# Performance work log

Measured on AMD Instinct MI355X. Metric: run time of the kernel, lower is better.

The kernel has to match this reference:

```python
import jax, jax.numpy as jnp
import numpy as np

EPS = 1e-12  # F.normalize default eps


def _unfold(x, k, pad, stride):
    # torch F.unfold: [B,C,H,W] -> [B, C*k*k, L], features ordered (c, kh, kw), L row-major.
    B, C, H, W = x.shape
    xp = jnp.pad(x, ((0, 0), (0, 0), (pad, pad), (pad, pad)))
    Ho = (H + 2 * pad - k) // stride + 1
    Wo = (W + 2 * pad - k) // stride + 1
    r = (jnp.arange(Ho) * stride)[:, None] + jnp.arange(k)[None, :]  # [Ho,k]
    c = (jnp.arange(Wo) * stride)[:, None] + jnp.arange(k)[None, :]  # [Wo,k]
    p = xp[:, :, r[:, None, :, None], c[None, :, None, :]]  # [B,C,Ho,Wo,k,k]
    return p.transpose(0, 1, 4, 5, 2, 3).reshape(B, C * k * k, Ho * Wo)


def _fold(p, out_hw, k, pad, stride):
    # torch F.fold: overlap-add inverse of _unfold.
    B, CKK, L = p.shape
    C = CKK // (k * k)
    H, W = out_hw
    Ho = (H + 2 * pad - k) // stride + 1
    Wo = (W + 2 * pad - k) // stride + 1
    p = p.reshape(B, C, k, k, Ho, Wo).transpose(0, 1, 4, 5, 2, 3)  # [B,C,Ho,Wo,k,k]
    r = (jnp.arange(Ho) * stride)[:, None] + jnp.arange(k)[None, :]
    c = (jnp.arange(Wo) * stride)[:, None] + jnp.arange(k)[None, :]
    out = jnp.zeros((B, C, H + 2 * pad, W + 2 * pad), p.dtype)
    out = out.at[:, :, r[:, None, :, None], c[None, :, None, :]].add(p)
    return out[:, :, pad:pad + H, pad:pad + W]


def _l2n(x, axis):
    n = jnp.sqrt(jnp.sum(x * x, axis=axis, keepdims=True))
    return x / jnp.maximum(n, EPS)


def setup_inputs() -> dict:
    key = jax.random.key(0)
    ks = jax.random.split(key, 11)
    B, H, W = 1, 32, 32
    f = jnp.float32
    return {
        'lrsr_lv3': jax.random.normal(ks[0], (B, 256, H, W), f),
        'refsr_lv1': jax.random.normal(ks[1], (B, 64, 4 * H, 4 * W), f),
        'refsr_lv2': jax.random.normal(ks[2], (B, 128, 2 * H, 2 * W), f),
        'refsr_lv3': jax.random.normal(ks[3], (B, 256, H, W), f),
        'ref_lv1': jax.random.normal(ks[4], (B, 64, 4 * H, 4 * W), f),
        'ref_lv2': jax.random.normal(ks[5], (B, 128, 2 * H, 2 * W), f),
        'ref_lv3': jax.random.normal(ks[6], (B, 256, H, W), f),
        'W1': jax.random.normal(ks[7], (2304, 1152), f) * 0.02,
        'b1': jax.random.normal(ks[8], (2304,), f) * 0.02,
        'W2': jax.random.normal(ks[9], (2304, 576), f) * 0.02,
        'b2': jax.random.normal(ks[10], (2304,), f) * 0.02,
    }


def reference(lrsr_lv3, refsr_lv1, refsr_lv2, refsr_lv3, ref_lv1, ref_lv2, ref_lv3, W1, b1, W2, b2):
    B, _, H, W = lrsr_lv3.shape
    lr3 = _unfold(lrsr_lv3, 3, 1, 1)                       # [B, 2304, N]
    r3 = _unfold(refsr_lv3, 3, 1, 1).transpose(0, 2, 1)    # [B, N3, 2304]
    r2 = _unfold(refsr_lv2, 3, 1, 1).transpose(0, 2, 1) @ W1.T + b1  # [B, N2, 2304]
    r1 = _unfold(refsr_lv1, 3, 1, 1).transpose(0, 2, 1) @ W2.T + b2  # [B, N1, 2304]
    r3 = _l2n(r3, 2); r2 = _l2n(r2, 2); r1 = _l2n(r1, 2)
    lr3 = _l2n(lr3, 1)
    R3 = jnp.einsum('bnd,bdm->bnm', r3, lr3)  # [B, N3, N]
    R2 = jnp.einsum('bnd,bdm->bnm', r2, lr3)  # [B, N2, N]
    R1 = jnp.einsum('bnd,bdm->bnm', r1, lr3)  # [B, N1, N]
    R3_star = jnp.max(R3, axis=1); R3_arg = jnp.argmax(R3, axis=1)
    R2_star = jnp.max(R2, axis=1)
    R1_star = jnp.max(R1, axis=1)
    ref3u = _unfold(ref_lv3, 3, 1, 1)
    ref2u = _unfold(ref_lv2, 6, 2, 2)
    ref1u = _unfold(ref_lv1, 12, 4, 4)
    idx = R3_arg[:, None, :]  # [B,1,N] broadcast over feature dim
    T3u = jnp.take_along_axis(ref3u, idx, axis=2)
    T2u = jnp.take_along_axis(ref2u, idx, axis=2)
    T1u = jnp.take_along_axis(ref1u, idx, axis=2)
    T_lv3 = _fold(T3u, (H, W), 3, 1, 1) / 9.0
    T_lv2 = _fold(T2u, (2 * H, 2 * W), 6, 2, 2) / 9.0
    T_lv1 = _fold(T1u, (4 * H, 4 * W), 12, 4, 4) / 9.0
    S_3 = R3_star.reshape(B, 1, H, W)
    S_2 = R2_star.reshape(B, 1, H, W)
    S_1 = R1_star.reshape(B, 1, H, W)
    return (S_1, S_2, S_3, T_lv3, T_lv2, T_lv1)
```

## Files before the change

### kernel.cpp

```cpp
#include <hip/hip_runtime.h>

typedef short bf8 __attribute__((ext_vector_type(8)));
typedef float f32x4 __attribute__((ext_vector_type(4)));

static __device__ __forceinline__ unsigned short f2bf(float f) {
  unsigned u = __float_as_uint(f);
  unsigned r = u + 0x7FFFu + ((u >> 16) & 1u);
  return (unsigned short)(r >> 16);
}
static __device__ __forceinline__ float bf2f(unsigned short h) {
  return __uint_as_float(((unsigned)h) << 16);
}
static __device__ __forceinline__ unsigned fkey(float f) {
  unsigned u = __float_as_uint(f);
  return (u & 0x80000000u) ? ~u : (u | 0x80000000u);
}
static __device__ __forceinline__ float kdec(unsigned k) {
  unsigned u = (k & 0x80000000u) ? (k & 0x7FFFFFFFu) : ~k;
  return __uint_as_float(u);
}
static __device__ __forceinline__ int xcdswz(int h, int nwg) {
  int q = nwg >> 3, r = nwg & 7;
  int xcd = h & 7, w = h >> 3;
  return (xcd < r ? xcd * (q + 1) : r * (q + 1) + (xcd - r) * q) + w;
}
static __device__ __forceinline__ int xcdbal(int h, int nwg, int nb0) {
  int xcd = h & 7, w = h >> 3;
  int qa = nb0 >> 3, qb = (nwg - nb0) >> 3;
  return (w < qa) ? (xcd * qa + w) : (nb0 + xcd * qb + (w - qa));
}
static __device__ __forceinline__ float win9s(const float* __restrict__ b, int m) {
  int mi = m >> 5, mj = m & 31;
  float s = 0.f;
#pragma unroll
  for (int dy = -1; dy <= 1; ++dy) {
    int i = mi + dy; if ((unsigned)i >= 32u) continue;
#pragma unroll
    for (int dx = -1; dx <= 1; ++dx) {
      int jx = mj + dx; if ((unsigned)jx >= 32u) continue;
      s += b[i * 32 + jx];
    }
  }
  return s;
}

static __device__ __forceinline__ void gload_lds16(const unsigned short* g, unsigned short* l) {
  __builtin_amdgcn_global_load_lds((const __attribute__((address_space(1))) void*)g,
                                   (__attribute__((address_space(3))) void*)l, 16, 0, 0);
}

static __device__ __forceinline__ float uf3(const float* __restrict__ src, int lgS, int d, int m) {
  const int S = 1 << lgS;
  int cc = d / 9;
  int r9 = d - cc * 9;
  int ki = r9 / 3;
  int kj = r9 - ki * 3;
  int i = (m >> lgS) + ki - 1;
  int j = (m & (S - 1)) + kj - 1;
  if ((unsigned)i >= (unsigned)S || (unsigned)j >= (unsigned)S) return 0.f;
  return src[((size_t)cc << (2 * lgS)) + ((size_t)i << lgS) + j];
}

__global__ __launch_bounds__(256) void k_prepA(const float* __restrict__ lrsr3, const float* __restrict__ rsr3,
                                               const float* __restrict__ rsr2, const float* __restrict__ rsr1,
                                               const float* __restrict__ W1, const float* __restrict__ W2,
                                               const float* __restrict__ b1, const float* __restrict__ b2,
                                               float* __restrict__ G2,
                                               float* __restrict__ rsr2t, float* __restrict__ rsr1t,
                                               unsigned short* __restrict__ lr3nbT,
                                               unsigned short* __restrict__ W1t, unsigned short* __restrict__ W2t,
                                               float* __restrict__ sclw, float* __restrict__ scu3w,
                                               float* __restrict__ D1, float* __restrict__ D2) {
  __shared__ __align__(16) unsigned char smem[18432];
  const int blk = blockIdx.x;
  const int tid = threadIdx.x;
  if (blk < 4) {
    float* b1L = (float*)smem;
    float* b2L = b1L + 2304;
    const int p = blk * 256 + tid;
    for (int i = tid; i < 2304; i += 256) { b1L[i] = b1[i]; b2L[i] = b2[i]; }
    __syncthreads();
    float d1a[9] = {}, d2a[9] = {};
    for (int cc = 0; cc < 256; ++cc) {
      float v = lrsr3[(size_t)cc * 1024 + p];
#pragma unroll
      for (int kk = 0; kk < 9; ++kk) {
        d1a[kk] = fmaf(b1L[cc * 9 + kk], v, d1a[kk]);
        d2a[kk] = fmaf(b2L[cc * 9 + kk], v, d2a[kk]);
      }
    }
#pragma unroll
    for (int kk = 0; kk < 9; ++kk) { D1[kk * 1024 + p] = d1a[kk]; D2[kk * 1024 + p] = d2a[kk]; }
  } else if (blk < 6) {
    float* ss = (float*)smem;
    const float* src = (blk == 4) ? lrsr3 : rsr3;
    float a4[4] = {0.f, 0.f, 0.f, 0.f};
    for (int cc = 0; cc < 256; ++cc) {
#pragma unroll
      for (int k = 0; k < 4; ++k) {
        float v = src[(size_t)cc * 1024 + k * 256 + tid];
        a4[k] = fmaf(v, v, a4[k]);
      }
    }
#pragma unroll
    for (int k = 0; k < 4; ++k) ss[k * 256 + tid] = a4[k];
    __syncthreads();
    float* dst = (blk == 4) ? sclw : scu3w;
#pragma unroll
    for (int k = 0; k < 4; ++k) {
      int m = k * 256 + tid;
      dst[m] = 1.f / fmaxf(sqrtf(win9s(ss, m)), 1e-12f);
    }
  } else if (blk < 1030) {
    float (*As)[32] = (float(*)[32])smem;
    float (*Bs)[32] = (float(*)[32])(smem + 2048);
    const int px = blk - 6;
    const int m0 = (px >> 5) * 32, n0 = (px & 31) * 32;
    const int tx = tid & 15, ty = tid >> 4;
    float acc[2][2] = {};
    for (int kb = 0; kb < 256; kb += 16) {
      __syncthreads();
      {
        int kk = tid >> 5, mm = tid & 31;
        As[kk][mm] = lrsr3[(size_t)(kb + kk) * 1024 + m0 + mm];
        Bs[kk][mm] = rsr3[(size_t)(kb + kk) * 1024 + n0 + mm];
        int e2 = tid + 256; int kk2 = e2 >> 5, mm2 = e2 & 31;
        As[kk2][mm2] = lrsr3[(size_t)(kb + kk2) * 1024 + m0 + mm2];
        Bs[kk2][mm2] = rsr3[(size_t)(kb + kk2) * 1024 + n0 + mm2];
      }
      __syncthreads();
#pragma unroll
      for (int kk = 0; kk < 16; ++kk) {
        float a0 = As[kk][ty * 2], a1 = As[kk][ty * 2 + 1];
        float b0 = Bs[kk][tx * 2], b1v = Bs[kk][tx * 2 + 1];
        acc[0][0] = fmaf(a0, b0, acc[0][0]); acc[0][1] = fmaf(a0, b1v, acc[0][1]);
        acc[1][0] = fmaf(a1, b0, acc[1][0]); acc[1][1] = fmaf(a1, b1v, acc[1][1]);
      }
    }
#pragma unroll
    for (int i = 0; i < 2; ++i)
#pragma unroll
      for (int jj = 0; jj < 2; ++jj)
        G2[(size_t)(m0 + ty * 2 + i) * 1024 + (n0 + tx * 2 + jj)] = acc[i][jj];
  } else if (blk < 1158) {
    float (*Tt)[65] = (float(*)[65])smem;
    const int idx = blk - 1030;
    const int ct = idx & 1, st = idx >> 1;
#pragma unroll
    for (int i = 0; i < 16; ++i) {
      int id = tid + i * 256;
      int r = id >> 6, c = id & 63;
      Tt[r][c] = rsr2[(size_t)(ct * 64 + r) * 4096 + st * 64 + c];
    }
    __syncthreads();
#pragma unroll
    for (int i = 0; i < 16; ++i) {
      int id = tid + i * 256;
      int cc2 = id >> 6, rr = id & 63;
      rsr2t[(size_t)(st * 64 + cc2) * 128 + ct * 64 + rr] = Tt[rr][cc2];
    }
  } else if (blk < 1414) {
    float (*Tt)[65] = (float(*)[65])smem;
    const int st = blk - 1158;
#pragma unroll
    for (int i = 0; i < 16; ++i) {
      int id = tid + i * 256;
      int r = id >> 6, c = id & 63;
      Tt[r][c] = rsr1[(size_t)r * 16384 + st * 64 + c];
    }
    __syncthreads();
#pragma unroll
    for (int i = 0; i < 16; ++i) {
      int id = tid + i * 256;
      int cc2 = id >> 6, rr = id & 63;
      rsr1t[(size_t)(st * 64 + cc2) * 64 + rr] = Tt[rr][cc2];
    }
  } else if (blk < 2566) {
    int id8 = (blk - 1414) * 256 + tid;
    int m = id8 / 288, c0 = (id8 - m * 288) * 8;
    bf8 v;
#pragma unroll
    for (int e = 0; e < 8; ++e) v[e] = (short)f2bf(uf3(lrsr3, 5, c0 + e, m));
    *(bf8*)(lr3nbT + (size_t)m * 2304 + c0) = v;
  } else {
    unsigned short (*Ls)[65] = (unsigned short(*)[65])smem;
    int idx = blk - 2566;
    int xx = idx % 27, yy = idx / 27;
    const float* W; unsigned short* Wt; int Cw, c0;
    if (xx < 18) { W = W1; Wt = W1t; Cw = 1152; c0 = xx * 64; }
    else         { W = W2; Wt = W2t; Cw = 576;  c0 = (xx - 18) * 64; }
    const int Cch = Cw / 9;
    const int d0 = yy * 64;
#pragma unroll
    for (int i = 0; i < 16; ++i) {
      int id = tid + i * 256;
      int r = id >> 6, c = id & 63;
      Ls[r][c] = f2bf(W[(size_t)(d0 + r) * Cw + c0 + c]);
    }
    __syncthreads();
#pragma unroll
    for (int i = 0; i < 16; ++i) {
      int id = tid + i * 256;
      int cc = id >> 6, rr = id & 63;
      int c = c0 + cc;
      Wt[(size_t)((c % 9) * Cch + c / 9) * 2304 + d0 + rr] = Ls[rr][cc];
    }
  }
}

struct Job {
  const unsigned short* Alo;
  const unsigned short* Ahi;
  const unsigned short* Bt;
  unsigned short* Clo;
  unsigned short* Chi;
  const float* bl;
  const float* bw;
  const float* bbp;
  const float* rowscale;
  float* pnsq;
  float* pbwd;
  float* cmax;
  int Msplit, N, K, nbx, Mtot, npart, which;
};

template <int EPI, int NBUF>
static __device__ __forceinline__ void gemm_body(const Job& j0, const Job& j1, int nb0, int bid,
                                                 unsigned char* smem) {
  unsigned short (*As)[128 * 64] = (unsigned short(*)[128 * 64])smem;
  unsigned short (*Bs)[128 * 64] = (unsigned short(*)[128 * 64])(smem + (size_t)NBUF * 16384);
  unsigned* colkey = (unsigned*)(smem + (size_t)2 * NBUF * 16384);
  float* ninvL = (float*)(smem + (size_t)2 * NBUF * 16384 + 512);

  const bool first = (bid < nb0);
  const Job j = first ? j0 : j1;
  const int local = bid - (first ? 0 : nb0);
  const int by = local / j.nbx;
  const int bx = local - by * j.nbx;
  const int m0 = by * 128, n0 = bx * 128;
  const int K = j.K, N = j.N;

  const unsigned short* Abase = (m0 < j.Msplit)
      ? j.Alo + (size_t)m0 * K
      : j.Ahi + (size_t)(m0 - j.Msplit) * K;

  const int tid = threadIdx.x;
  const int l = tid & 63;
  const int w = tid >> 6;
  const int wr = w >> 1, wc = w & 1;
  if (EPI == 2) {
    if (tid < 128) {
      colkey[tid] = 0u;
      const int r = m0 + tid;
      float nsq = 0.f, bwd = 0.f;
      for (int p = 0; p < j.npart; ++p) {
        nsq += j.pnsq[(size_t)p * j.Mtot + r];
        bwd += j.pbwd[(size_t)p * j.Mtot + r];
      }
      float tq = nsq + 2.f * bwd + j.bbp[j.which];
      ninvL[tid] = 1.f / fmaxf(sqrtf(fmaxf(tq, 0.f)), 1e-12f);
    }
  }

  f32x4 acc[4][4] = {};

  const int srow = w * 32;
  const int lrow = l >> 3;
  const int gcol = ((l & 7) ^ lrow) * 8;
  const int mr = l & 15;
  const int kg = l >> 4;

  const int nt = K >> 6;
  const int snap_kb = n0 + wc * 64;
  unsigned short snap[4][4][4];

  auto stage = [&](int buf, int kb) {
#pragma unroll
    for (int i = 0; i < 4; ++i) {
      int r = srow + i * 8;
      gload_lds16(Abase + (size_t)(r + lrow) * K + kb + gcol, &As[buf][r * 64]);
      gload_lds16(j.Bt + (size_t)(n0 + r + lrow) * K + kb + gcol, &Bs[buf][r * 64]);
    }
  };
  auto compute_tile = [&](int cur) {
#pragma unroll
    for (int ks = 0; ks < 2; ++ks) {
      bf8 af[4], bv[4];
#pragma unroll
      for (int mi = 0; mi < 4; ++mi) {
        const int row = wr * 64 + mi * 16 + mr;
        af[mi] = *(const bf8*)&As[cur][row * 64 + (((ks * 4 + kg) ^ (row & 7)) * 8)];
      }
#pragma unroll
      for (int ni = 0; ni < 4; ++ni) {
        const int row = wc * 64 + ni * 16 + mr;
        bv[ni] = *(const bf8*)&Bs[cur][row * 64 + (((ks * 4 + kg) ^ (row & 7)) * 8)];
      }
      __builtin_amdgcn_s_setprio(1);
#pragma unroll
      for (int mi = 0; mi < 4; ++mi)
#pragma unroll
        for (int ni = 0; ni < 4; ++ni)
          acc[mi][ni] = __builtin_amdgcn_mfma_f32_16x16x32_bf16(af[mi], bv[ni], acc[mi][ni], 0, 0, 0);
      __builtin_amdgcn_s_setprio(0);
    }
  };
  auto do_snap = [&](int cur) {
#pragma unroll
    for (int mi = 0; mi < 4; ++mi)
#pragma unroll
      for (int e = 0; e < 4; ++e) {
        const int row = wr * 64 + mi * 16 + kg * 4 + e;
#pragma unroll
        for (int ni = 0; ni < 4; ++ni) {
          const int slot = ni * 2 + (mr >> 3);
          snap[mi][ni][e] = As[cur][row * 64 + ((slot ^ (row & 7)) * 8) + (mr & 7)];
        }
      }
  };

  if constexpr (NBUF == 1) {
    for (int t = 0; t < nt; ++t) {
      if (t) __syncthreads();
      stage(0, t << 6);
      __syncthreads();
      compute_tile(0);
      if (EPI == 1 && (t << 6) == snap_kb) do_snap(0);
    }
  } else {
    auto waitv = [&](int Wt) {
      if (Wt >= 2)      asm volatile("s_waitcnt vmcnt(16)\ns_barrier" ::: "memory");
      else if (Wt == 1) asm volatile("s_waitcnt vmcnt(8)\ns_barrier" ::: "memory");
      else              asm volatile("s_waitcnt vmcnt(0)\ns_barrier" ::: "memory");
    };
#pragma unroll
    for (int p = 0; p < NBUF; ++p) if (p < nt) stage(p, p << 6);
    { int inflight = (NBUF < nt ? NBUF : nt); waitv(inflight - 1); }
    int cur = 0;
    for (int t = 0; t < nt; ++t) {
      compute_tile(cur);
      if (EPI == 1 && (t << 6) == snap_kb) do_snap(cur);
      if (t + 1 < nt) {
        asm volatile("s_waitcnt lgkmcnt(0)\ns_barrier" ::: "memory");
        if (t + NBUF < nt) stage(cur, (t + NBUF) << 6);
        const int im = (nt - 1 < t + NBUF) ? (nt - 1) : (t + NBUF);
        waitv(im - (t + 1));
        cur = (cur + 1 == NBUF) ? 0 : cur + 1;
      }
    }
  }

  const int lr0 = wr * 64;
  const int lc0 = wc * 64;
  if (EPI == 0) {
    const bool hi = (m0 >= j.Msplit);
    unsigned short* Cbase = hi ? j.Chi + (size_t)(m0 - j.Msplit) * N
                               : j.Clo + (size_t)m0 * N;
    float rs[4][4];
#pragma unroll
    for (int mi = 0; mi < 4; ++mi)
#pragma unroll
      for (int e = 0; e < 4; ++e)
        rs[mi][e] = hi ? j.rowscale[m0 - j.Msplit + lr0 + mi * 16 + kg * 4 + e] : 1.f;
#pragma unroll
    for (int mi = 0; mi < 4; ++mi)
#pragma unroll
      for (int ni = 0; ni < 4; ++ni)
#pragma unroll
        for (int e = 0; e < 4; ++e)
          Cbase[(size_t)(lr0 + mi * 16 + kg * 4 + e) * (size_t)N + (n0 + lc0 + ni * 16 + mr)] =
              f2bf(acc[mi][ni][e] * rs[mi][e]);
  } else if (EPI == 1) {
    float rp[4][4] = {};
    float bp[4][4] = {};
#pragma unroll
    for (int ni = 0; ni < 4; ++ni) {
      const float bwv = j.bw[n0 + lc0 + ni * 16 + mr];
#pragma unroll
      for (int mi = 0; mi < 4; ++mi)
#pragma unroll
        for (int e = 0; e < 4; ++e) {
          const float av = bf2f(snap[mi][ni][e]);
          rp[mi][e] += acc[mi][ni][e] * av;
          bp[mi][e] += bwv * av;
        }
    }
#pragma unroll
    for (int off = 1; off < 16; off <<= 1)
#pragma unroll
      for (int mi = 0; mi < 4; ++mi)
#pragma unroll
        for (int e = 0; e < 4; ++e) {
          rp[mi][e] += __shfl_xor(rp[mi][e], off);
          bp[mi][e] += __shfl_xor(bp[mi][e], off);
        }
    if (mr == 0) {
      const size_t slotbase = (size_t)(bx * 2 + wc) * j.Mtot;
#pragma unroll
      for (int mi = 0; mi < 4; ++mi)
#pragma unroll
        for (int e = 0; e < 4; ++e) {
          const int r = m0 + lr0 + mi * 16 + kg * 4 + e;
          j.pnsq[slotbase + r] = rp[mi][e];
          j.pbwd[slotbase + r] = bp[mi][e];
        }
    }
  } else {
    float nv[4][4];
#pragma unroll
    for (int mi = 0; mi < 4; ++mi)
#pragma unroll
      for (int e = 0; e < 4; ++e)
        nv[mi][e] = ninvL[lr0 + mi * 16 + kg * 4 + e];
#pragma unroll
    for (int ni = 0; ni < 4; ++ni) {
      float blv = j.bl[n0 + lc0 + ni * 16 + mr];
      float mx = -3.0e38f;
#pragma unroll
      for (int mi = 0; mi < 4; ++mi)
#pragma unroll
        for (int e = 0; e < 4; ++e) mx = fmaxf(mx, (acc[mi][ni][e] + blv) * nv[mi][e]);
      atomicMax(&colkey[lc0 + ni * 16 + mr], fkey(mx));
    }
    __syncthreads();
    if (tid < 128) j.cmax[(size_t)by * 1024 + n0 + tid] = kdec(colkey[tid]);
  }
}

__global__ __launch_bounds__(256) void k_prepBP(Job pa, Job pb, int nbP0,
                                                const float* __restrict__ rsr2t, const float* __restrict__ rsr1t,
                                                const float* __restrict__ W1, const float* __restrict__ W2,
                                                const float* __restrict__ b1, const float* __restrict__ b2,
                                                const float* __restrict__ sclw, const float* __restrict__ scu3w,
                                                const float* __restrict__ D1, const float* __restrict__ D2,
                                                const float* __restrict__ G2,
                                                unsigned short* __restrict__ U2b, unsigned short* __restrict__ U1b,
                                                float* __restrict__ bw2, float* __restrict__ bw1,
                                                float* __restrict__ bb,
                                                float* __restrict__ bl2, float* __restrict__ bl1,
                                                float* __restrict__ s3, int* __restrict__ arg) {
  __shared__ __align__(16) unsigned char sm[33792];
  const int blk = blockIdx.x;
  const int tid = threadIdx.x;
  if (blk < 218) {
    gemm_body<0, 1>(pa, pb, nbP0, xcdswz(blk, 218), sm);
  } else if (blk < 2522) {
    int id = (blk - 218) * 256 + tid;
    int t = id & 15, rest = id >> 4;
    int kk = rest % 9, n = rest / 9;
    int cc0 = t * 8;
    int ki = kk / 3, kj = kk - ki * 3;
    int sy = (n >> 6) + ki - 1, sx = (n & 63) + kj - 1;
    bf8 v;
    if ((unsigned)sy < 64u && (unsigned)sx < 64u) {
      const float* p = rsr2t + (size_t)(sy * 64 + sx) * 128 + cc0;
      f32x4 a = *(const f32x4*)p;
      f32x4 bq = *(const f32x4*)(p + 4);
#pragma unroll
      for (int e = 0; e < 4; ++e) { v[e] = (short)f2bf(a[e]); v[4 + e] = (short)f2bf(bq[e]); }
    } else {
#pragma unroll
      for (int e = 0; e < 8; ++e) v[e] = 0;
    }
    *(bf8*)(U2b + (size_t)n * 1152 + kk * 128 + cc0) = v;
  } else if (blk < 7642) {
    int id = (blk - 2522) * 256 + tid;
    int n = id / 80, rem = id - n * 80;
    int ks = rem >> 3, t = rem & 7;
    int cc0 = t * 8;
    bf8 v;
    if (ks == 9) {
#pragma unroll
      for (int e = 0; e < 8; ++e) v[e] = 0;
    } else {
      int ki = ks / 3, kj = ks - ki * 3;
      int sy = (n >> 7) + ki - 1, sx = (n & 127) + kj - 1;
      if ((unsigned)sy < 128u && (unsigned)sx < 128u) {
        const float* p = rsr1t + (size_t)(sy * 128 + sx) * 64 + cc0;
        f32x4 a = *(const f32x4*)p;
        f32x4 bq = *(const f32x4*)(p + 4);
#pragma unroll
        for (int e = 0; e < 4; ++e) { v[e] = (short)f2bf(a[e]); v[4 + e] = (short)f2bf(bq[e]); }
      } else {
#pragma unroll
        for (int e = 0; e < 8; ++e) v[e] = 0;
      }
    }
    *(bf8*)(U1b + (size_t)n * 640 + ks * 64 + cc0) = v;
  } else if (blk < 7722) {
    float* red = (float*)sm;
    int idx = blk - 7642;
    int x = idx & 7, y = idx >> 3;
    if (y == 9) {
      if (x >= 2) return;
      const float* b = x ? b2 : b1;
      float s = 0.f;
      for (int d = tid; d < 2304; d += 256) s += b[d] * b[d];
      red[tid] = s; __syncthreads();
      for (int o = 128; o > 0; o >>= 1) { if (tid < o) red[tid] += red[tid + o]; __syncthreads(); }
      if (tid == 0) bb[x] = red[0];
      return;
    }
    const bool two = x < 5;
    const float* W = two ? W1 : W2;
    const float* b = two ? b1 : b2;
    float* bw = two ? bw2 : bw1;
    const int Cw = two ? 1152 : 576;
    int c = (two ? x : x - 5) * 256 + tid;
    if (c >= Cw) return;
    int d0 = y * 256;
    float s = 0.f;
    for (int d = d0; d < d0 + 256; ++d) s += b[d] * W[(size_t)d * Cw + c];
    atomicAdd(&bw[(c % 9) * (Cw / 9) + c / 9], s);
  } else if (blk < 8746) {
    float* bv = (float*)sm;
    int* bidx = (int*)(sm + 1024);
    const int m = blk - 7722;
    const int mi = m >> 5, mj = m & 31;
    float best = -3.0e38f; int bi = 0;
    for (int n = tid; n < 1024; n += 256) {
      const int ni = n >> 5, nj = n & 31;
      float raw = 0.f;
#pragma unroll
      for (int dy = -1; dy <= 1; ++dy) {
#pragma unroll
        for (int dx = -1; dx <= 1; ++dx) {
          bool vm = ((unsigned)(mi + dy) < 32u) && ((unsigned)(mj + dx) < 32u);
          bool vn = ((unsigned)(ni + dy) < 32u) && ((unsigned)(nj + dx) < 32u);
          if (vm && vn) {
            int off = dy * 32 + dx;
            raw += G2[(size_t)(m + off) * 1024 + (n + off)];
          }
        }
      }
      float v = raw * scu3w[n];
      if (v > best) { best = v; bi = n; }
    }
    bv[tid] = best; bidx[tid] = bi;
    __syncthreads();
    for (int o = 128; o > 0; o >>= 1) {
      if (tid < o) {
        float ov = bv[tid + o]; int oi = bidx[tid + o];
        if (ov > bv[tid] || (ov == bv[tid] && oi < bidx[tid])) { bv[tid] = ov; bidx[tid] = oi; }
      }
      __syncthreads();
    }
    if (tid == 0) { s3[m] = bv[0] * sclw[m]; arg[m] = bidx[0]; }
  } else {
    int m = (blk - 8746) * 256 + tid;
    int mi = m >> 5, mj = m & 31;
    float a1 = 0.f, a2 = 0.f;
#pragma unroll
    for (int ki = 0; ki < 3; ++ki) {
      int i = mi + ki - 1; if ((unsigned)i >= 32u) continue;
#pragma unroll
      for (int kj = 0; kj < 3; ++kj) {
        int jx = mj + kj - 1; if ((unsigned)jx >= 32u) continue;
        int pix = i * 32 + jx;
        int kk = ki * 3 + kj;
        a1 += D1[kk * 1024 + pix];
        a2 += D2[kk * 1024 + pix];
      }
    }
    float sc = sclw[m];
    bl2[m] = a1 * sc;
    bl1[m] = a2 * sc;
  }
}

__global__ __launch_bounds__(256) void k_gE1F(Job a, Job b, int nb0,
                                              const float* __restrict__ ref3, const float* __restrict__ ref2,
                                              const float* __restrict__ ref1, const int* __restrict__ arg,
                                              float* __restrict__ out) {
  __shared__ __align__(16) unsigned char sm[33792];
  const int bid = blockIdx.x;
  const int tid = threadIdx.x;
  if (bid < 928) {
    gemm_body<1, 1>(a, b, nb0, xcdbal(bid, 928, nb0), sm);
  } else if (bid < 1184) {
    float* plane = (float*)sm;
    int* argL = (int*)(sm + 4096);
    const int c = bid - 928;
#pragma unroll
    for (int k = 0; k < 4; ++k) {
      plane[k * 256 + tid] = ref3[(size_t)c * 1024 + k * 256 + tid];
      argL[k * 256 + tid] = arg[k * 256 + tid];
    }
    __syncthreads();
#pragma unroll
    for (int k = 0; k < 4; ++k) {
      int px = k * 256 + tid;
      int y = px >> 5, x = px & 31;
      float s = 0.f;
#pragma unroll
      for (int di = -1; di <= 1; ++di) {
        int i = y + di;
        if ((unsigned)i >= 32u) continue;
#pragma unroll
        for (int dj = -1; dj <= 1; ++dj) {
          int jw = x + dj;
          if ((unsigned)jw >= 32u) continue;
          int n2 = argL[i * 32 + jw];
          int rr = (n2 >> 5) + y - i, cc = (n2 & 31) + x - jw;
          if ((unsigned)rr < 32u && (unsigned)cc < 32u) s += plane[rr * 32 + cc];
        }
      }
      out[3072 + (size_t)c * 1024 + px] = s * (1.f / 9.f);
    }
  } else if (bid < 2208) {
    int* argL = (int*)sm;
#pragma unroll
    for (int k = 0; k < 4; ++k) argL[k * 256 + tid] = arg[k * 256 + tid];
    __syncthreads();
    int id2 = (bid - 1184) * 256 + tid;
    int q = id2 & 31, y = (id2 >> 5) & 63, c = id2 >> 11;
    int iy = y >> 1;
    float s0 = 0.f, s1 = 0.f;
#pragma unroll
    for (int di = -1; di <= 1; ++di) {
      int i = iy + di;
      if ((unsigned)i >= 32u) continue;
      int ry = y - 2 * i;
#pragma unroll
      for (int dj = -1; dj <= 1; ++dj) {
        int jw = q + dj;
        if ((unsigned)jw >= 32u) continue;
        int n2 = argL[i * 32 + jw];
        int rr = (n2 >> 5) * 2 + ry;
        int cb = (n2 & 31) * 2 + 2 * (q - jw);
        if ((unsigned)rr < 64u && (unsigned)cb < 63u) {
          const float* p = ref2 + (size_t)c * 4096 + rr * 64 + cb;
          s0 += p[0]; s1 += p[1];
        }
      }
    }
    float2 o; o.x = s0 * (1.f / 9.f); o.y = s1 * (1.f / 9.f);
    *(float2*)(out + 265216 + (size_t)c * 4096 + y * 64 + 2 * q) = o;
  } else {
    int* argL = (int*)sm;
#pragma unroll
    for (int k = 0; k < 4; ++k) argL[k * 256 + tid] = arg[k * 256 + tid];
    __syncthreads();
    int id1 = (bid - 2208) * 256 + tid;
    int q = id1 & 31, y = (id1 >> 5) & 127, c = id1 >> 12;
    int iy = y >> 2;
    f32x4 s = {0.f, 0.f, 0.f, 0.f};
#pragma unroll
    for (int di = -1; di <= 1; ++di) {
      int i = iy + di;
      if ((unsigned)i >= 32u) continue;
      int ry = y - 4 * i;
#pragma unroll
      for (int dj = -1; dj <= 1; ++dj) {
        int jw = q + dj;
        if ((unsigned)jw >= 32u) continue;
        int n2 = argL[i * 32 + jw];
        int rr = (n2 >> 5) * 4 + ry;
        int cb = (n2 & 31) * 4 + 4 * (q - jw);
        if ((unsigned)rr < 128u && (unsigned)cb < 125u) {
          f32x4 v = *(const f32x4*)(ref1 + (size_t)c * 16384 + rr * 128 + cb);
          s += v;
        }
      }
    }
    s *= (1.f / 9.f);
    *(f32x4*)(out + 789504 + (size_t)c * 16384 + y * 128 + 4 * q) = s;
  }
}

__global__ __launch_bounds__(256) void k_gE2(Job a, Job b, int nb0) {
  __shared__ __align__(16) unsigned char sm[33792];
  gemm_body<2, 1>(a, b, nb0, xcdbal((int)blockIdx.x, (int)gridDim.x, nb0), sm);
}

__global__ __launch_bounds__(256) void k_sfin(const float* __restrict__ cmax1, const float* __restrict__ cmax2,
                                              float* __restrict__ out) {
  int t = blockIdx.x * 256 + threadIdx.x;
  if (t < 1024) {
    float mx = -3.0e38f;
    for (int rb = 0; rb < 128; ++rb) mx = fmaxf(mx, cmax1[rb * 1024 + t]);
    out[t] = mx;
  } else {
    int tt = t - 1024;
    float mx = -3.0e38f;
    for (int rb = 0; rb < 32; ++rb) mx = fmaxf(mx, cmax2[rb * 1024 + tt]);
    out[1024 + tt] = mx;
  }
}

static constexpr size_t OFF_BW2     = 0;
static constexpr size_t OFF_BW1     = 4608;
static constexpr size_t ZERO_BYTES  = 7168;
static constexpr size_t OFF_BB      = 7168;
static constexpr size_t OFF_BL2     = 7424;
static constexpr size_t OFF_BL1     = 11520;
static constexpr size_t OFF_SCLW    = 15616;
static constexpr size_t OFF_SCU3W   = 19712;
static constexpr size_t OFF_R3ARG   = 23808;
static constexpr size_t OFF_PNSQ2   = 27904;
static constexpr size_t OFF_PBWD2   = OFF_PNSQ2 + 294912;
static constexpr size_t OFF_PNSQ1   = OFF_PBWD2 + 294912;
static constexpr size_t OFF_PBWD1   = OFF_PNSQ1 + 655360;
static constexpr size_t OFF_CMAX2   = OFF_PBWD1 + 655360;
static constexpr size_t OFF_CMAX1   = OFF_CMAX2 + 131072;
static constexpr size_t OFF_LR3NBT  = OFF_CMAX1 + 524288;
static constexpr size_t OFF_U2B     = OFF_LR3NBT + 4718592;
static constexpr size_t OFF_U1B     = OFF_U2B    + 9437184;
static constexpr size_t OFF_W1T     = OFF_U1B    + 20971520;
static constexpr size_t OFF_W2T     = OFF_W1T    + 5308416;
static constexpr size_t OFF_A2      = OFF_W2T    + 2949120;
static constexpr size_t OFF_A1      = OFF_A2     + 2654208;
static constexpr size_t OFF_M2T     = OFF_A1     + 819200;
static constexpr size_t OFF_M1T     = OFF_M2T    + 2359296;
static constexpr size_t OFF_G2      = OFF_M1T    + 1310720;
static constexpr size_t OFF_R2T     = OFF_G2     + 4194304;
static constexpr size_t OFF_R1T     = OFF_R2T    + 2097152;
static constexpr size_t OFF_D1      = OFF_R1T    + 4194304;
static constexpr size_t OFF_D2      = OFF_D1     + 36864;

extern "C" void kernel_launch(void* const* d_in, const int* in_sizes, int n_in,
                              void* d_out, int out_size, void* d_ws, size_t ws_size,
                              hipStream_t stream) {
  (void)in_sizes; (void)n_in; (void)out_size; (void)ws_size;
  const float* lrsr3  = (const float*)d_in[0];
  const float* rsr1   = (const float*)d_in[1];
  const float* rsr2   = (const float*)d_in[2];
  const float* rsr3   = (const float*)d_in[3];
  const float* ref1   = (const float*)d_in[4];
  const float* ref2   = (const float*)d_in[5];
  const float* ref3   = (const float*)d_in[6];
  const float* W1     = (const float*)d_in[7];
  const float* b1     = (const float*)d_in[8];
  const float* W2     = (const float*)d_in[9];
  const float* b2     = (const float*)d_in[10];
  float* out = (float*)d_out;
  char* ws = (char*)d_ws;

  float*          bw2     = (float*)(ws + OFF_BW2);
  float*          bw1     = (float*)(ws + OFF_BW1);
  float*          bb      = (float*)(ws + OFF_BB);
  float*          bl2     = (float*)(ws + OFF_BL2);
  float*          bl1     = (float*)(ws + OFF_BL1);
  float*          sclw    = (float*)(ws + OFF_SCLW);
  float*          scu3w   = (float*)(ws + OFF_SCU3W);
  int*            R3arg   = (int*)(ws + OFF_R3ARG);
  float*          pnsq2   = (float*)(ws + OFF_PNSQ2);
  float*          pbwd2   = (float*)(ws + OFF_PBWD2);
  float*          pnsq1   = (float*)(ws + OFF_PNSQ1);
  float*          pbwd1   = (float*)(ws + OFF_PBWD1);
  float*          cmax2   = (float*)(ws + OFF_CMAX2);
  float*          cmax1   = (float*)(ws + OFF_CMAX1);
  unsigned short* lr3nbT  = (unsigned short*)(ws + OFF_LR3NBT);
  unsigned short* U2b     = (unsigned short*)(ws + OFF_U2B);
  unsigned short* U1b     = (unsigned short*)(ws + OFF_U1B);
  unsigned short* W1t     = (unsigned short*)(ws + OFF_W1T);
  unsigned short* W2t     = (unsigned short*)(ws + OFF_W2T);
  unsigned short* A2b     = (unsigned short*)(ws + OFF_A2);
  unsigned short* A1b     = (unsigned short*)(ws + OFF_A1);
  unsigned short* M2tb    = (unsigned short*)(ws + OFF_M2T);
  unsigned short* M1tb    = (unsigned short*)(ws + OFF_M1T);
  float*          G2      = (float*)(ws + OFF_G2);
  float*          rsr2t   = (float*)(ws + OFF_R2T);
  float*          rsr1t   = (float*)(ws + OFF_R1T);
  float*          D1      = (float*)(ws + OFF_D1);
  float*          D2      = (float*)(ws + OFF_D2);

  hipMemsetAsync(d_ws, 0, ZERO_BYTES, stream);
  hipMemsetAsync(ws + OFF_W2T + (size_t)576 * 2304 * 2, 0, (size_t)64 * 2304 * 2, stream);

  k_prepA<<<3538, 256, 0, stream>>>(lrsr3, rsr3, rsr2, rsr1, W1, W2, b1, b2,
                                    G2, rsr2t, rsr1t, lr3nbT, W1t, W2t, sclw, scu3w, D1, D2);

  Job jz = {};
  {
    Job a = jz, b = jz;
    a.Alo = W1t; a.Ahi = lr3nbT; a.Msplit = 1152; a.Bt = W1t;
    a.Clo = A2b; a.Chi = M2tb; a.rowscale = sclw; a.N = 1152; a.K = 2304; a.nbx = 9;
    b.Alo = W2t; b.Ahi = lr3nbT; b.Msplit = 640; b.Bt = W2t;
    b.Clo = A1b; b.Chi = M1tb; b.rowscale = sclw; b.N = 640; b.K = 2304; b.nbx = 5;
    k_prepBP<<<8750, 256, 0, stream>>>(a, b, 153, rsr2t, rsr1t, W1, W2, b1, b2,
                                       sclw, scu3w, D1, D2, G2,
                                       U2b, U1b, bw2, bw1, bb, bl2, bl1, out + 2048, R3arg);
  }
  {
    Job a = jz, b = jz;
    a.Alo = U2b; a.Ahi = U2b; a.Msplit = 4096; a.Bt = A2b;
    a.bw = bw2; a.pnsq = pnsq2; a.pbwd = pbwd2; a.Mtot = 4096;
    a.N = 1152; a.K = 1152; a.nbx = 9;
    b.Alo = U1b; b.Ahi = U1b; b.Msplit = 16384; b.Bt = A1b;
    b.bw = bw1; b.pnsq = pnsq1; b.pbwd = pbwd1; b.Mtot = 16384;
    b.N = 640; b.K = 640; b.nbx = 5;
    k_gE1F<<<3232, 256, 0, stream>>>(a, b, 288, ref3, ref2, ref1, R3arg, out);
  }
  {
    Job a = jz, b = jz;
    a.Alo = U2b; a.Ahi = U2b; a.Msplit = 4096; a.Bt = M2tb;
    a.bl = bl2; a.pnsq = pnsq2; a.pbwd = pbwd2; a.bbp = bb;
    a.npart = 18; a.which = 0; a.cmax = cmax2; a.Mtot = 4096;
    a.N = 1024; a.K = 1152; a.nbx = 8;
    b.Alo = U1b; b.Ahi = U1b; b.Msplit = 16384; b.Bt = M1tb;
    b.bl = bl1; b.pnsq = pnsq1; b.pbwd = pbwd1; b.bbp = bb;
    b.npart = 10; b.which = 1; b.cmax = cmax1; b.Mtot = 16384;
    b.N = 1024; b.K = 640; b.nbx = 8;
    k_gE2<<<256 + 1024, 256, 0, stream>>>(a, b, 256);
  }

  k_sfin<<<8, 256, 0, stream>>>(cmax1, cmax2, out);
}
```

Before: 208.9 us.

## Split-K the weight Gram GEMM in prepBP with fp32 atomics and a combine kernel

The K=2304 weight-product GEMM inside k_prepBP is split into two K halves, doubling its block count from 218 to 436, to raise parallelism for this long-K tail. Each half atomically adds fp32 partials into a new zeroed workspace. A new k_pcomb kernel then applies the row scale and converts to bf16 for the downstream GEMMs. In exchange it adds a memset of about 14 MB, atomic traffic, an extra kernel launch and fp32 partial reads and writes. It also removes the unused multi-buffer pipeline path from gemm_body.

```diff
diff --git a/kernel.cpp b/kernel.cpp
--- a/kernel.cpp
+++ b/kernel.cpp
@@ -212,21 +212,19 @@
   const unsigned short* Alo;
   const unsigned short* Ahi;
   const unsigned short* Bt;
-  unsigned short* Clo;
-  unsigned short* Chi;
   const float* bl;
   const float* bw;
   const float* bbp;
-  const float* rowscale;
+  float* Fp;
   float* pnsq;
   float* pbwd;
   float* cmax;
-  int Msplit, N, K, nbx, Mtot, npart, which;
+  int Msplit, N, K, Kst, nbx, Mtot, npart, which;
 };
 
 template <int EPI, int NBUF>
 static __device__ __forceinline__ void gemm_body(const Job& j0, const Job& j1, int nb0, int bid,
-                                                 unsigned char* smem) {
+                                                 unsigned char* smem, int k0) {
   unsigned short (*As)[128 * 64] = (unsigned short(*)[128 * 64])smem;
   unsigned short (*Bs)[128 * 64] = (unsigned short(*)[128 * 64])(smem + (size_t)NBUF * 16384);
   unsigned* colkey = (unsigned*)(smem + (size_t)2 * NBUF * 16384);
@@ -238,11 +236,11 @@
   const int by = local / j.nbx;
   const int bx = local - by * j.nbx;
   const int m0 = by * 128, n0 = bx * 128;
-  const int K = j.K, N = j.N;
+  const int K = j.K, Kst = j.Kst, N = j.N;
 
   const unsigned short* Abase = (m0 < j.Msplit)
-      ? j.Alo + (size_t)m0 * K
-      : j.Ahi + (size_t)(m0 - j.Msplit) * K;
+      ? j.Alo + (size_t)m0 * Kst
+      : j.Ahi + (size_t)(m0 - j.Msplit) * Kst;
 
   const int tid = threadIdx.x;
   const int l = tid & 63;
@@ -278,8 +276,8 @@
 #pragma unroll
     for (int i = 0; i < 4; ++i) {
       int r = srow + i * 8;
-      gload_lds16(Abase + (size_t)(r + lrow) * K + kb + gcol, &As[buf][r * 64]);
-      gload_lds16(j.Bt + (size_t)(n0 + r + lrow) * K + kb + gcol, &Bs[buf][r * 64]);
+      gload_lds16(Abase + (size_t)(r + lrow) * Kst + k0 + kb + gcol, &As[buf][r * 64]);
+      gload_lds16(j.Bt + (size_t)(n0 + r + lrow) * Kst + k0 + kb + gcol, &Bs[buf][r * 64]);
     }
   };
   auto compute_tile = [&](int cur) {
@@ -319,57 +317,26 @@
       }
   };
 
-  if constexpr (NBUF == 1) {
-    for (int t = 0; t < nt; ++t) {
-      if (t) __syncthreads();
-      stage(0, t << 6);
-      __syncthreads();
-      compute_tile(0);
-      if (EPI == 1 && (t << 6) == snap_kb) do_snap(0);
-    }
-  } else {
-    auto waitv = [&](int Wt) {
-      if (Wt >= 2)      asm volatile("s_waitcnt vmcnt(16)\ns_barrier" ::: "memory");
-      else if (Wt == 1) asm volatile("s_waitcnt vmcnt(8)\ns_barrier" ::: "memory");
-      else              asm volatile("s_waitcnt vmcnt(0)\ns_barrier" ::: "memory");
-    };
-#pragma unroll
-    for (int p = 0; p < NBUF; ++p) if (p < nt) stage(p, p << 6);
-    { int inflight = (NBUF < nt ? NBUF : nt); waitv(inflight - 1); }
-    int cur = 0;
-    for (int t = 0; t < nt; ++t) {
-      compute_tile(cur);
-      if (EPI == 1 && (t << 6) == snap_kb) do_snap(cur);
-      if (t + 1 < nt) {
-        asm volatile("s_waitcnt lgkmcnt(0)\ns_barrier" ::: "memory");
-        if (t + NBUF < nt) stage(cur, (t + NBUF) << 6);
-        const int im = (nt - 1 < t + NBUF) ? (nt - 1) : (t + NBUF);
-        waitv(im - (t + 1));
-        cur = (cur + 1 == NBUF) ? 0 : cur + 1;
-      }
-    }
+  for (int t = 0; t < nt; ++t) {
+    if (t) __syncthreads();
+    stage(0, t << 6);
+    __syncthreads();
+    compute_tile(0);
+    if (EPI == 1 && (t << 6) == snap_kb) do_snap(0);
   }
 
   const int lr0 = wr * 64;
   const int lc0 = wc * 64;
-  if (EPI == 0) {
-    const bool hi = (m0 >= j.Msplit);
-    unsigned short* Cbase = hi ? j.Chi + (size_t)(m0 - j.Msplit) * N
-                               : j.Clo + (size_t)m0 * N;
-    float rs[4][4];
+  if (EPI == 3) {
+    float* F = j.Fp + (size_t)m0 * N;
 #pragma unroll
     for (int mi = 0; mi < 4; ++mi)
 #pragma unroll
-      for (int e = 0; e < 4; ++e)
-        rs[mi][e] = hi ? j.rowscale[m0 - j.Msplit + lr0 + mi * 16 + kg * 4 + e] : 1.f;
-#pragma unroll
-    for (int mi = 0; mi < 4; ++mi)
-#pragma unroll
       for (int ni = 0; ni < 4; ++ni)
 #pragma unroll
         for (int e = 0; e < 4; ++e)
-          Cbase[(size_t)(lr0 + mi * 16 + kg * 4 + e) * (size_t)N + (n0 + lc0 + ni * 16 + mr)] =
-              f2bf(acc[mi][ni][e] * rs[mi][e]);
+          atomicAdd(&F[(size_t)(lr0 + mi * 16 + kg * 4 + e) * (size_t)N + (n0 + lc0 + ni * 16 + mr)],
+                    acc[mi][ni][e]);
   } else if (EPI == 1) {
     float rp[4][4] = {};
     float bp[4][4] = {};
@@ -442,10 +409,12 @@
   __shared__ __align__(16) unsigned char sm[33792];
   const int blk = blockIdx.x;
   const int tid = threadIdx.x;
-  if (blk < 218) {
-    gemm_body<0, 1>(pa, pb, nbP0, xcdswz(blk, 218), sm);
-  } else if (blk < 2522) {
-    int id = (blk - 218) * 256 + tid;
+  if (blk < 436) {
+    const int h = blk / 218;
+    const int inner = blk - h * 218;
+    gemm_body<3, 1>(pa, pb, nbP0, xcdswz(inner, 218), sm, h * 1152);
+  } else if (blk < 2740) {
+    int id = (blk - 436) * 256 + tid;
     int t = id & 15, rest = id >> 4;
     int kk = rest % 9, n = rest / 9;
     int cc0 = t * 8;
@@ -463,8 +432,8 @@
       for (int e = 0; e < 8; ++e) v[e] = 0;
     }
     *(bf8*)(U2b + (size_t)n * 1152 + kk * 128 + cc0) = v;
-  } else if (blk < 7642) {
-    int id = (blk - 2522) * 256 + tid;
+  } else if (blk < 7860) {
+    int id = (blk - 2740) * 256 + tid;
     int n = id / 80, rem = id - n * 80;
     int ks = rem >> 3, t = rem & 7;
     int cc0 = t * 8;
@@ -487,9 +456,9 @@
       }
     }
     *(bf8*)(U1b + (size_t)n * 640 + ks * 64 + cc0) = v;
-  } else if (blk < 7722) {
+  } else if (blk < 7940) {
     float* red = (float*)sm;
-    int idx = blk - 7642;
+    int idx = blk - 7860;
     int x = idx & 7, y = idx >> 3;
     if (y == 9) {
       if (x >= 2) return;
@@ -512,10 +481,10 @@
     float s = 0.f;
     for (int d = d0; d < d0 + 256; ++d) s += b[d] * W[(size_t)d * Cw + c];
     atomicAdd(&bw[(c % 9) * (Cw / 9) + c / 9], s);
-  } else if (blk < 8746) {
+  } else if (blk < 8964) {
     float* bv = (float*)sm;
     int* bidx = (int*)(sm + 1024);
-    const int m = blk - 7722;
+    const int m = blk - 7940;
     const int mi = m >> 5, mj = m & 31;
     float best = -3.0e38f; int bi = 0;
     for (int n = tid; n < 1024; n += 256) {
@@ -547,7 +516,7 @@
     }
     if (tid == 0) { s3[m] = bv[0] * sclw[m]; arg[m] = bidx[0]; }
   } else {
-    int m = (blk - 8746) * 256 + tid;
+    int m = (blk - 8964) * 256 + tid;
     int mi = m >> 5, mj = m & 31;
     float a1 = 0.f, a2 = 0.f;
 #pragma unroll
@@ -565,6 +534,37 @@
     float sc = sclw[m];
     bl2[m] = a1 * sc;
     bl1[m] = a2 * sc;
+  }
+}
+
+__global__ __launch_bounds__(256) void k_pcomb(const float* __restrict__ PPa, const float* __restrict__ PPb,
+                                               const float* __restrict__ sclw,
+                                               unsigned short* __restrict__ A2b, unsigned short* __restrict__ M2tb,
+                                               unsigned short* __restrict__ A1b, unsigned short* __restrict__ M1tb) {
+  const int blk = blockIdx.x;
+  const int tid = threadIdx.x;
+  if (blk < 1224) {
+    int e8 = blk * 256 + tid;
+    int row = e8 / 144, c0 = (e8 - row * 144) * 8;
+    const float* p = PPa + (size_t)row * 1152 + c0;
+    float sc = (row < 1152) ? 1.f : sclw[row - 1152];
+    unsigned short* dst = (row < 1152) ? (A2b + (size_t)row * 1152 + c0)
+                                       : (M2tb + (size_t)(row - 1152) * 1152 + c0);
+    bf8 v;
+#pragma unroll
+    for (int e = 0; e < 8; ++e) v[e] = (short)f2bf(p[e] * sc);
+    *(bf8*)dst = v;
+  } else {
+    int e8 = (blk - 1224) * 256 + tid;
+    int row = e8 / 80, c0 = (e8 - row * 80) * 8;
+    const float* p = PPb + (size_t)row * 640 + c0;
+    float sc = (row < 640) ? 1.f : sclw[row - 640];
+    unsigned short* dst = (row < 640) ? (A1b + (size_t)row * 640 + c0)
+                                      : (M1tb + (size_t)(row - 640) * 640 + c0);
+    bf8 v;
+#pragma unroll
+    for (int e = 0; e < 8; ++e) v[e] = (short)f2bf(p[e] * sc);
+    *(bf8*)dst = v;
   }
 }
 
@@ -576,7 +576,7 @@
   const int bid = blockIdx.x;
   const int tid = threadIdx.x;
   if (bid < 928) {
-    gemm_body<1, 1>(a, b, nb0, xcdbal(bid, 928, nb0), sm);
+    gemm_body<1, 1>(a, b, nb0, xcdbal(bid, 928, nb0), sm, 0);
   } else if (bid < 1184) {
     float* plane = (float*)sm;
     int* argL = (int*)(sm + 4096);
@@ -670,7 +670,7 @@
 
 __global__ __launch_bounds__(256) void k_gE2(Job a, Job b, int nb0) {
   __shared__ __align__(16) unsigned char sm[33792];
-  gemm_body<2, 1>(a, b, nb0, xcdbal((int)blockIdx.x, (int)gridDim.x, nb0), sm);
+  gemm_body<2, 1>(a, b, nb0, xcdbal((int)blockIdx.x, (int)gridDim.x, nb0), sm, 0);
 }
 
 __global__ __launch_bounds__(256) void k_sfin(const float* __restrict__ cmax1, const float* __restrict__ cmax2,
@@ -717,6 +717,9 @@
 static constexpr size_t OFF_R1T     = OFF_R2T    + 2097152;
 static constexpr size_t OFF_D1      = OFF_R1T    + 4194304;
 static constexpr size_t OFF_D2      = OFF_D1     + 36864;
+static constexpr size_t OFF_PPA     = OFF_D2     + 36864;
+static constexpr size_t OFF_PPB     = OFF_PPA    + 10027008;
+static constexpr size_t PP_BYTES    = 10027008 + 4259840;
 
 extern "C" void kernel_launch(void* const* d_in, const int* in_sizes, int n_in,
                               void* d_out, int out_size, void* d_ws, size_t ws_size,
@@ -764,8 +767,11 @@
   float*          rsr1t   = (float*)(ws + OFF_R1T);
   float*          D1      = (float*)(ws + OFF_D1);
   float*          D2      = (float*)(ws + OFF_D2);
+  float*          PPa     = (float*)(ws + OFF_PPA);
+  float*          PPb     = (float*)(ws + OFF_PPB);
 
   hipMemsetAsync(d_ws, 0, ZERO_BYTES, stream);
+  hipMemsetAsync(ws + OFF_PPA, 0, PP_BYTES, stream);
   hipMemsetAsync(ws + OFF_W2T + (size_t)576 * 2304 * 2, 0, (size_t)64 * 2304 * 2, stream);
 
   k_prepA<<<3538, 256, 0, stream>>>(lrsr3, rsr3, rsr2, rsr1, W1, W2, b1, b2,
@@ -775,21 +781,22 @@
   {
     Job a = jz, b = jz;
     a.Alo = W1t; a.Ahi = lr3nbT; a.Msplit = 1152; a.Bt = W1t;
-    a.Clo = A2b; a.Chi = M2tb; a.rowscale = sclw; a.N = 1152; a.K = 2304; a.nbx = 9;
+    a.Fp = PPa; a.N = 1152; a.K = 1152; a.Kst = 2304; a.nbx = 9;
     b.Alo = W2t; b.Ahi = lr3nbT; b.Msplit = 640; b.Bt = W2t;
-    b.Clo = A1b; b.Chi = M1tb; b.rowscale = sclw; b.N = 640; b.K = 2304; b.nbx = 5;
-    k_prepBP<<<8750, 256, 0, stream>>>(a, b, 153, rsr2t, rsr1t, W1, W2, b1, b2,
+    b.Fp = PPb; b.N = 640; b.K = 1152; b.Kst = 2304; b.nbx = 5;
+    k_prepBP<<<8968, 256, 0, stream>>>(a, b, 153, rsr2t, rsr1t, W1, W2, b1, b2,
                                        sclw, scu3w, D1, D2, G2,
                                        U2b, U1b, bw2, bw1, bb, bl2, bl1, out + 2048, R3arg);
   }
+  k_pcomb<<<1744, 256, 0, stream>>>(PPa, PPb, sclw, A2b, M2tb, A1b, M1tb);
   {
     Job a = jz, b = jz;
     a.Alo = U2b; a.Ahi = U2b; a.Msplit = 4096; a.Bt = A2b;
     a.bw = bw2; a.pnsq = pnsq2; a.pbwd = pbwd2; a.Mtot = 4096;
-    a.N = 1152; a.K = 1152; a.nbx = 9;
+    a.N = 1152; a.K = 1152; a.Kst = 1152; a.nbx = 9;
     b.Alo = U1b; b.Ahi = U1b; b.Msplit = 16384; b.Bt = A1b;
     b.bw = bw1; b.pnsq = pnsq1; b.pbwd = pbwd1; b.Mtot = 16384;
-    b.N = 640; b.K = 640; b.nbx = 5;
+    b.N = 640; b.K = 640; b.Kst = 640; b.nbx = 5;
     k_gE1F<<<3232, 256, 0, stream>>>(a, b, 288, ref3, ref2, ref1, R3arg, out);
   }
   {
@@ -797,11 +804,11 @@
     a.Alo = U2b; a.Ahi = U2b; a.Msplit = 4096; a.Bt = M2tb;
     a.bl = bl2; a.pnsq = pnsq2; a.pbwd = pbwd2; a.bbp = bb;
     a.npart = 18; a.which = 0; a.cmax = cmax2; a.Mtot = 4096;
-    a.N = 1024; a.K = 1152; a.nbx = 8;
+    a.N = 1024; a.K = 1152; a.Kst = 1152; a.nbx = 8;
     b.Alo = U1b; b.Ahi = U1b; b.Msplit = 16384; b.Bt = M1tb;
     b.bl = bl1; b.pnsq = pnsq1; b.pbwd = pbwd1; b.bbp = bb;
     b.npart = 10; b.which = 1; b.cmax = cmax1; b.Mtot = 16384;
-    b.N = 1024; b.K = 640; b.nbx = 8;
+    b.N = 1024; b.K = 640; b.Kst = 640; b.nbx = 8;
     k_gE2<<<256 + 1024, 256, 0, stream>>>(a, b, 256);
   }
 
```

Result: slower. 233.7 us (+11.9%).
